# Kernel tuning notes

Measured on AMD Instinct MI355X. Metric: run time of the kernel, lower is better.

The kernel has to match this reference:

```python
import jax, jax.numpy as jnp
import numpy as np

B, S, D, H = 2, 2048, 1024, 16
DH = D // H

def setup_inputs() -> dict:
    key = jax.random.key(0)
    ks = jax.random.split(key, 9)
    s = 1.0 / np.sqrt(D)
    def lin(k):
        kw, kb = jax.random.split(k)
        W = jax.random.uniform(kw, (D, D), jnp.float32, -s, s)
        b = jax.random.uniform(kb, (D,), jnp.float32, -s, s)
        return W, b
    Wq, bq = lin(ks[0]); Wk, bk = lin(ks[1]); Wv, bv = lin(ks[2]); Wo, bo = lin(ks[3])
    x = jax.random.normal(ks[4], (B, S, D), jnp.float32)
    return {"x": x, "Wq": Wq, "bq": bq, "Wk": Wk, "bk": bk,
            "Wv": Wv, "bv": bv, "Wo": Wo, "bo": bo}

def _split_heads(t):
    # [B,S,D] -> [B,H,S,DH]
    return t.reshape(B, S, H, DH).transpose(0, 2, 1, 3)

def reference(x, Wq, bq, Wk, bk, Wv, bv, Wo, bo):
    # torch Linear: y = x @ W.T + b
    q = _split_heads(x @ Wq.T + bq)
    k = _split_heads(x @ Wk.T + bk)
    v = _split_heads(x @ Wv.T + bv)
    scores = jnp.einsum('bhqd,bhkd->bhqk', q, k) / jnp.sqrt(jnp.float32(DH))
    p = jax.nn.softmax(scores, axis=-1)  # dropout is identity in eval
    o = jnp.einsum('bhqk,bhkd->bhqd', p, v)
    o = o.transpose(0, 2, 1, 3).reshape(B, S, D)  # combine heads
    return o @ Wo.T + bo
```

## Files before the change

kernel.cpp:

```cpp
#include <hip/hip_runtime.h>


typedef __bf16 bf16;
typedef bf16 bf16x8 __attribute__((ext_vector_type(8)));
typedef bf16 bf16x4 __attribute__((ext_vector_type(4)));
typedef short s16x4 __attribute__((ext_vector_type(4)));
typedef float f32x4 __attribute__((ext_vector_type(4)));

#define MFMA32(a, b, c) __builtin_amdgcn_mfma_f32_16x16x32_bf16(a, b, c, 0, 0, 0)

#if __has_builtin(__builtin_amdgcn_mfma_f32_16x16x16bf16_1k)
#define HAVE_MFMA16 1
#define MFMA16(a, b, c) __builtin_amdgcn_mfma_f32_16x16x16bf16_1k(a, b, c, 0, 0, 0)
#else
#define HAVE_MFMA16 0
#endif

#define GLL(g, l) __builtin_amdgcn_global_load_lds(                              \
    (const __attribute__((address_space(1))) void*)(const void*)(g),             \
    (__attribute__((address_space(3))) void*)(void*)(l), 16, 0, 0)

union pk4 { bf16x4 h; s16x4 s; unsigned int d[2]; };

__global__ __launch_bounds__(256)
void cvt_bf16(const float* __restrict__ x,  const float* __restrict__ Wq,
              const float* __restrict__ Wk, const float* __restrict__ Wv,
              const float* __restrict__ Wo,
              bf16* __restrict__ xb, bf16* __restrict__ wqb, bf16* __restrict__ wkb,
              bf16* __restrict__ wvb, bf16* __restrict__ wob)
{
    const int idx = blockIdx.x * 256 + threadIdx.x;
    const float* src; bf16* dst; int off;
    if (idx < 1048576) { src = x; dst = xb; off = idx; }
    else {
        const int r = idx - 1048576;
        const int seg = r >> 18;
        off = r & 262143;
        src = (seg == 0) ? Wq : (seg == 1) ? Wk : (seg == 2) ? Wv : Wo;
        dst = (seg == 0) ? wqb : (seg == 1) ? wkb : (seg == 2) ? wvb : wob;
    }
    const float4 v = ((const float4*)src)[off];
    bf16x4 o = {(bf16)v.x, (bf16)v.y, (bf16)v.z, (bf16)v.w};
    *(bf16x4*)(dst + (size_t)off * 4) = o;
}

__global__ __launch_bounds__(256, 3)
void qkv_gemm(const bf16* __restrict__ xb,
              const bf16* __restrict__ wqb, const float* __restrict__ bq,
              const bf16* __restrict__ wkb, const float* __restrict__ bk,
              const bf16* __restrict__ wvb, const float* __restrict__ bv,
              bf16* __restrict__ q_ws, bf16* __restrict__ k_ws, bf16* __restrict__ v_ws)
{
    const int z = blockIdx.z;
    const bf16*  W    = (z == 0) ? wqb : (z == 1) ? wkb : wvb;
    const float* bias = (z == 0) ? bq  : (z == 1) ? bk  : bv;

    __shared__ bf16 As[128][64];
    __shared__ bf16 Bs[128][64];
    __shared__ char ebuf[17408];
    bf16 (*Et)[68]  = (bf16(*)[68])ebuf;
    bf16 (*Vt)[132] = (bf16(*)[132])ebuf;

    const int m0 = blockIdx.x * 128;
    const int n0 = blockIdx.y * 128;
    const int t    = threadIdx.x;
    const int wave = t >> 6;
    const int lane = t & 63;
    const int lr   = lane & 15;
    const int quad = lane >> 4;
    const int wm = (wave & 1) * 64;
    const int wn = (wave >> 1) * 64;

    const int srow8 = lane >> 3;
    const int pcol  = (lane & 7) * 8;
    const int gcol  = ((lane & 7) ^ (lane >> 3)) * 8;
    const bf16* gaU[4]; const bf16* gbU[4]; bf16* laU[4]; bf16* lbU[4];
    #pragma unroll
    for (int u = 0; u < 4; u++) {
        const int row = wave * 32 + u * 8 + srow8;
        gaU[u] = xb + (size_t)(m0 + row) * 1024 + gcol;
        gbU[u] = W  + (size_t)(n0 + row) * 1024 + gcol;
        laU[u] = &As[row][pcol];
        lbU[u] = &Bs[row][pcol];
    }
    const int swA = (lr & 7) * 8;

    f32x4 acc[4][4] = {};

    for (int k0 = 0; k0 < 1024; k0 += 64) {
        #pragma unroll
        for (int u = 0; u < 4; u++) {
            GLL(gaU[u] + k0, laU[u]);
            GLL(gbU[u] + k0, lbU[u]);
        }
        __syncthreads();

        bf16x8 af[4][2], bfr[4][2];
        #pragma unroll
        for (int i = 0; i < 4; i++)
            #pragma unroll
            for (int kc = 0; kc < 2; kc++)
                af[i][kc] = *(const bf16x8*)&As[wm + i*16 + lr][(kc*32 + quad*8) ^ swA];
        #pragma unroll
        for (int j = 0; j < 4; j++)
            #pragma unroll
            for (int kc = 0; kc < 2; kc++)
                bfr[j][kc] = *(const bf16x8*)&Bs[wn + j*16 + lr][(kc*32 + quad*8) ^ swA];
        #pragma unroll
        for (int kc = 0; kc < 2; kc++)
            #pragma unroll
            for (int i = 0; i < 4; i++)
                #pragma unroll
                for (int j = 0; j < 4; j++)
                    acc[i][j] = MFMA32(af[i][kc], bfr[j][kc], acc[i][j]);
        __syncthreads();
    }

    const int bi = m0 >> 11, si0 = m0 & 2047;
    if (z < 2) {
        bf16* hw = (z == 0) ? q_ws : k_ws;
        const float sc = (z == 0) ? 0.125f : 1.0f;
        #pragma unroll
        for (int ph = 0; ph < 2; ph++) {
            if ((wave >> 1) == ph) {
                #pragma unroll
                for (int j = 0; j < 4; j++) {
                    const float bb = bias[n0 + ph * 64 + j * 16 + lr];
                    #pragma unroll
                    for (int i = 0; i < 4; i++)
                        #pragma unroll
                        for (int r = 0; r < 4; r++)
                            Et[wm + i*16 + quad*4 + r][j*16 + lr] =
                                (bf16)((acc[i][j][r] + bb) * sc);
                }
            }
            __syncthreads();
            const int hh = (n0 >> 6) + ph;
            bf16* dst = hw + (((size_t)bi * 16 + hh) * 2048 + si0) * 64;
            const int row = t >> 1, cc = (t & 1) * 32;
            #pragma unroll
            for (int e = 0; e < 4; e++)
                *(bf16x8*)(dst + (size_t)row * 64 + cc + e * 8) =
                    *(const bf16x8*)&Et[row][cc + e * 8];
            __syncthreads();
        }
    } else {
        #pragma unroll
        for (int ph = 0; ph < 2; ph++) {
            if ((wave >> 1) == ph) {
                #pragma unroll
                for (int j = 0; j < 4; j++) {
                    const float bb = bias[n0 + ph * 64 + j * 16 + lr];
                    #pragma unroll
                    for (int i = 0; i < 4; i++)
                        #pragma unroll
                        for (int r = 0; r < 4; r++)
                            Vt[j * 16 + lr][wm + i * 16 + quad * 4 + r] =
                                (bf16)(acc[i][j][r] + bb);
                }
            }
            __syncthreads();
            const int c  = t >> 2;
            const int sc_ = (t & 3) * 32;
            const int col = n0 + ph * 64 + c;
            const int h = col >> 6, dh = col & 63;
            bf16* dst = v_ws + (((size_t)bi * 16 + h) * 64 + dh) * 2048 + si0 + sc_;
            #pragma unroll
            for (int e = 0; e < 4; e++)
                *(bf16x8*)(dst + e * 8) = *(const bf16x8*)&Vt[c][sc_ + e * 8];
            __syncthreads();
        }
    }
}

__global__ __launch_bounds__(512, 4)
void attn(const bf16* __restrict__ q_ws, const bf16* __restrict__ k_ws,
          const bf16* __restrict__ v_ws, bf16* __restrict__ o_ws)
{
    const int bh = blockIdx.x;
    const int qt = blockIdx.y;
    const int b_ = bh >> 4, h = bh & 15;

    const bf16* qbase = q_ws + (size_t)bh * 2048 * 64;
    const bf16* kbase = k_ws + (size_t)bh * 2048 * 64;
    const bf16* vbase = v_ws + (size_t)bh * 64 * 2048;

    __shared__ bf16 Ks[128][72];
    __shared__ bf16 Vs[64][140];

    const int t    = threadIdx.x;
    const int wave = t >> 6;
    const int lane = t & 63;
    const int lr   = lane & 15;
    const int quad = lane >> 4;

    bf16x8 aq[2];
    #pragma unroll
    for (int kc = 0; kc < 2; kc++)
        aq[kc] = *(const bf16x8*)(qbase +
            (size_t)(qt*128 + wave*16 + lr) * 64 + kc*32 + quad*8);

    float m_i = -1e30f, l_i = 0.f;
    f32x4 o_accT[4] = {};
    const float C = 1.44269504f;

    bf16x8 kreg[2], vreg[2];
    #pragma unroll
    for (int u = 0; u < 2; u++) {
        const int c = t + u * 512;
        kreg[u] = *(const bf16x8*)(kbase + (size_t)c * 8);
        vreg[u] = *(const bf16x8*)(vbase + (size_t)(c >> 4) * 2048 + (c & 15) * 8);
    }

    for (int kt = 0; kt < 16; kt++) {
        __syncthreads();
        #pragma unroll
        for (int u = 0; u < 2; u++) {
            const int c = t + u * 512;
            *(bf16x8*)&Ks[c >> 3][(c & 7) * 8]  = kreg[u];
            *(bf16x8*)&Vs[c >> 4][(c & 15) * 8] = vreg[u];
        }
        __syncthreads();
        if (kt < 15) {
            #pragma unroll
            for (int u = 0; u < 2; u++) {
                const int c = t + u * 512;
                kreg[u] = *(const bf16x8*)(kbase + (size_t)(kt+1) * 8192 + c * 8);
                vreg[u] = *(const bf16x8*)(vbase + (size_t)(c >> 4) * 2048
                                           + (kt+1) * 128 + (c & 15) * 8);
            }
        }

        f32x4 sacc[8];
        #pragma unroll
        for (int j = 0; j < 8; j++) {
            bf16x8 kf0 = *(const bf16x8*)&Ks[j*16 + lr][quad*8];
            bf16x8 kf1 = *(const bf16x8*)&Ks[j*16 + lr][32 + quad*8];
            f32x4 a = {0.f, 0.f, 0.f, 0.f};
            a = MFMA32(kf0, aq[0], a);
            a = MFMA32(kf1, aq[1], a);
            sacc[j] = a;
        }

        float m = -1e30f;
        #pragma unroll
        for (int j = 0; j < 8; j++)
            #pragma unroll
            for (int r = 0; r < 4; r++) m = fmaxf(m, sacc[j][r]);
        m = fmaxf(m, __shfl_xor(m, 16));
        m = fmaxf(m, __shfl_xor(m, 32));
        const float nm = fmaxf(m_i, m);
        const float al = exp2f((m_i - nm) * C);
        m_i = nm;
        const float nmc = nm * C;
        float rs = 0.f;
        #pragma unroll
        for (int j = 0; j < 8; j++)
            #pragma unroll
            for (int r = 0; r < 4; r++) {
                const float p = exp2f(fmaf(sacc[j][r], C, -nmc));
                sacc[j][r] = p;
                rs += p;
            }
        #pragma unroll
        for (int n = 0; n < 4; n++)
            #pragma unroll
            for (int r = 0; r < 4; r++) o_accT[n][r] *= al;
        rs += __shfl_xor(rs, 16);
        rs += __shfl_xor(rs, 32);
        l_i = l_i * al + rs;

#if HAVE_MFMA16
        #pragma unroll
        for (int j = 0; j < 8; j++) {
            pk4 pf;
            pf.h = bf16x4{(bf16)sacc[j][0], (bf16)sacc[j][1],
                          (bf16)sacc[j][2], (bf16)sacc[j][3]};
            #pragma unroll
            for (int fb = 0; fb < 4; fb++) {
                pk4 vf;
                *(unsigned long long*)vf.d =
                    *(const unsigned long long*)&Vs[fb*16 + lr][j*16 + quad*4];
                o_accT[fb] = MFMA16(vf.s, pf.s, o_accT[fb]);
            }
        }
#else
        unsigned int p0[8], p1[8];
        #pragma unroll
        for (int j = 0; j < 8; j++) {
            pk4 pf;
            pf.h = bf16x4{(bf16)sacc[j][0], (bf16)sacc[j][1],
                          (bf16)sacc[j][2], (bf16)sacc[j][3]};
            p0[j] = pf.d[0]; p1[j] = pf.d[1];
        }
        const int srcA = lr + 32 * (quad & 1);
        const int srcB = srcA + 16;
        const bool hi = (quad >> 1) != 0;
        #pragma unroll
        for (int c = 0; c < 4; c++) {
            unsigned int a0 = __shfl(p0[2*c], srcA), a1 = __shfl(p0[2*c+1], srcA);
            unsigned int b0 = __shfl(p1[2*c], srcA), b1 = __shfl(p1[2*c+1], srcA);
            unsigned int c0 = __shfl(p0[2*c], srcB), c1 = __shfl(p0[2*c+1], srcB);
            unsigned int d0 = __shfl(p1[2*c], srcB), d1 = __shfl(p1[2*c+1], srcB);
            unsigned int fr[4];
            fr[0] = hi ? a1 : a0;
            fr[1] = hi ? b1 : b0;
            fr[2] = hi ? c1 : c0;
            fr[3] = hi ? d1 : d0;
            bf16x8 pf8 = *(bf16x8*)fr;
            #pragma unroll
            for (int fb = 0; fb < 4; fb++) {
                bf16x8 vf8 = *(const bf16x8*)&Vs[fb*16 + lr][c*32 + quad*8];
                o_accT[fb] = MFMA32(vf8, pf8, o_accT[fb]);
            }
        }
#endif
    }

    __syncthreads();
    bf16 (*OsE)[68] = (bf16(*)[68])&Ks[0][0];
    const float inv = 1.0f / l_i;
    const int sil = wave * 16 + lr;
    #pragma unroll
    for (int fb = 0; fb < 4; fb++)
        #pragma unroll
        for (int r = 0; r < 4; r++)
            OsE[sil][fb*16 + quad*4 + r] = (bf16)(o_accT[fb][r] * inv);
    __syncthreads();
    const int row = t >> 2, seg = (t & 3) * 16;
    bf16* dst = o_ws + ((size_t)b_ * 2048 + qt*128 + row) * 1024 + h*64 + seg;
    *(bf16x8*)(dst)     = *(const bf16x8*)&OsE[row][seg];
    *(bf16x8*)(dst + 8) = *(const bf16x8*)&OsE[row][seg + 8];
}

__global__ __launch_bounds__(256, 3)
void out_gemm(const bf16* __restrict__ o_ws,
              const bf16* __restrict__ wob, const float* __restrict__ bo,
              float* __restrict__ out)
{
    __shared__ bf16 As[64][64];
    __shared__ bf16 Bs[128][64];
    __shared__ float Ot[64][68];

    const int m0 = blockIdx.x * 64;
    const int n0 = blockIdx.y * 128;
    const int t    = threadIdx.x;
    const int wave = t >> 6;
    const int lane = t & 63;
    const int lr   = lane & 15;
    const int quad = lane >> 4;
    const int wm = (wave & 1) * 32;
    const int wn = (wave >> 1) * 64;

    const int srow8 = lane >> 3;
    const int pcol  = (lane & 7) * 8;
    const int gcol  = ((lane & 7) ^ (lane >> 3)) * 8;
    const bf16* gaU[2]; bf16* laU[2];
    #pragma unroll
    for (int u = 0; u < 2; u++) {
        const int row = wave * 16 + u * 8 + srow8;
        gaU[u] = o_ws + (size_t)(m0 + row) * 1024 + gcol;
        laU[u] = &As[row][pcol];
    }
    const bf16* gbU[4]; bf16* lbU[4];
    #pragma unroll
    for (int u = 0; u < 4; u++) {
        const int row = wave * 32 + u * 8 + srow8;
        gbU[u] = wob + (size_t)(n0 + row) * 1024 + gcol;
        lbU[u] = &Bs[row][pcol];
    }
    const int swA = (lr & 7) * 8;

    f32x4 acc[2][4] = {};

    for (int k0 = 0; k0 < 1024; k0 += 64) {
        #pragma unroll
        for (int u = 0; u < 2; u++) GLL(gaU[u] + k0, laU[u]);
        #pragma unroll
        for (int u = 0; u < 4; u++) GLL(gbU[u] + k0, lbU[u]);
        __syncthreads();

        bf16x8 af[2][2], bfr[4][2];
        #pragma unroll
        for (int i = 0; i < 2; i++)
            #pragma unroll
            for (int kc = 0; kc < 2; kc++)
                af[i][kc] = *(const bf16x8*)&As[wm + i*16 + lr][(kc*32 + quad*8) ^ swA];
        #pragma unroll
        for (int j = 0; j < 4; j++)
            #pragma unroll
            for (int kc = 0; kc < 2; kc++)
                bfr[j][kc] = *(const bf16x8*)&Bs[wn + j*16 + lr][(kc*32 + quad*8) ^ swA];
        #pragma unroll
        for (int kc = 0; kc < 2; kc++)
            #pragma unroll
            for (int i = 0; i < 2; i++)
                #pragma unroll
                for (int j = 0; j < 4; j++)
                    acc[i][j] = MFMA32(af[i][kc], bfr[j][kc], acc[i][j]);
        __syncthreads();
    }

    #pragma unroll
    for (int ph = 0; ph < 2; ph++) {
        if ((wave >> 1) == ph) {
            #pragma unroll
            for (int j = 0; j < 4; j++) {
                const float bb = bo[n0 + ph * 64 + j * 16 + lr];
                #pragma unroll
                for (int i = 0; i < 2; i++)
                    #pragma unroll
                    for (int r = 0; r < 4; r++)
                        Ot[wm + i*16 + quad*4 + r][j*16 + lr] = acc[i][j][r] + bb;
            }
        }
        __syncthreads();
        const int row = t >> 2, seg = (t & 3) * 16;
        float* dst = out + (size_t)(m0 + row) * 1024 + n0 + ph * 64 + seg;
        #pragma unroll
        for (int e = 0; e < 4; e++)
            *(float4*)(dst + e * 4) = *(const float4*)&Ot[row][seg + e * 4];
        __syncthreads();
    }
}

extern "C" void kernel_launch(void* const* d_in, const int* in_sizes, int n_in,
                              void* d_out, int out_size, void* d_ws, size_t ws_size,
                              hipStream_t stream) {
    (void)in_sizes; (void)n_in; (void)out_size; (void)ws_size;
    const float* x  = (const float*)d_in[0];
    const float* Wq = (const float*)d_in[1];
    const float* bq = (const float*)d_in[2];
    const float* Wk = (const float*)d_in[3];
    const float* bk = (const float*)d_in[4];
    const float* Wv = (const float*)d_in[5];
    const float* bv = (const float*)d_in[6];
    const float* Wo = (const float*)d_in[7];
    const float* bo = (const float*)d_in[8];
    float* out = (float*)d_out;

    char* ws = (char*)d_ws;
    const size_t MB = 1024 * 1024;
    bf16* xb   = (bf16*)(ws);
    bf16* wqb  = (bf16*)(ws + 8 * MB);
    bf16* wkb  = (bf16*)(ws + 10 * MB);
    bf16* wvb  = (bf16*)(ws + 12 * MB);
    bf16* wob  = (bf16*)(ws + 14 * MB);
    bf16* q_ws = (bf16*)(ws + 16 * MB);
    bf16* k_ws = (bf16*)(ws + 24 * MB);
    bf16* v_ws = (bf16*)(ws + 32 * MB);
    bf16* o_ws = (bf16*)(ws + 40 * MB);

    hipLaunchKernelGGL(cvt_bf16, dim3(8192), dim3(256), 0, stream,
                       x, Wq, Wk, Wv, Wo, xb, wqb, wkb, wvb, wob);
    hipLaunchKernelGGL(qkv_gemm, dim3(32, 8, 3), dim3(256), 0, stream,
                       xb, wqb, bq, wkb, bk, wvb, bv, q_ws, k_ws, v_ws);
    hipLaunchKernelGGL(attn, dim3(32, 16), dim3(512), 0, stream,
                       q_ws, k_ws, v_ws, o_ws);
    hipLaunchKernelGGL(out_gemm, dim3(64, 8), dim3(256), 0, stream,
                       o_ws, wob, bo, out);
}
```

Measured before the change: 212.7 us.

## Double query rows per wave and double-buffer K/V tiles in attention

Each wave now handles two 16-row query subtiles, so every K/V fragment read from LDS feeds twice as many MFMAs. The attention grid shrinks to 8 query tiles of 256 rows. K/V LDS staging is double-buffered with register prefetch two tiles ahead, which drops one barrier per iteration. In exchange it doubles accumulator registers and LDS use, lowers launch-bounds occupancy to 2, and halves the number of blocks (256), which may underfill the GPU.

```diff
diff --git a/kernel.cpp b/kernel.cpp
--- a/kernel.cpp
+++ b/kernel.cpp
@@ -173,7 +173,7 @@
     }
 }
 
-__global__ __launch_bounds__(512, 4)
+__global__ __launch_bounds__(512, 2)
 void attn(const bf16* __restrict__ q_ws, const bf16* __restrict__ k_ws,
           const bf16* __restrict__ v_ws, bf16* __restrict__ o_ws)
 {
@@ -185,8 +185,8 @@
     const bf16* kbase = k_ws + (size_t)bh * 2048 * 64;
     const bf16* vbase = v_ws + (size_t)bh * 64 * 2048;
 
-    __shared__ bf16 Ks[128][72];
-    __shared__ bf16 Vs[64][140];
+    __shared__ bf16 KsB[2 * 128 * 72];
+    __shared__ bf16 VsB[2 * 64 * 140];
 
     const int t    = threadIdx.x;
     const int wave = t >> 6;
@@ -194,143 +194,171 @@
     const int lr   = lane & 15;
     const int quad = lane >> 4;
 
-    bf16x8 aq[2];
-    #pragma unroll
-    for (int kc = 0; kc < 2; kc++)
-        aq[kc] = *(const bf16x8*)(qbase +
-            (size_t)(qt*128 + wave*16 + lr) * 64 + kc*32 + quad*8);
-
-    float m_i = -1e30f, l_i = 0.f;
-    f32x4 o_accT[4] = {};
+    bf16x8 aq[2][2];
+    #pragma unroll
+    for (int s = 0; s < 2; s++)
+        #pragma unroll
+        for (int kc = 0; kc < 2; kc++)
+            aq[s][kc] = *(const bf16x8*)(qbase +
+                (size_t)(qt*256 + wave*32 + s*16 + lr) * 64 + kc*32 + quad*8);
+
+    float m_i[2] = {-1e30f, -1e30f}, l_i[2] = {0.f, 0.f};
+    f32x4 o_accT[2][4] = {};
     const float C = 1.44269504f;
 
+    const int c0 = t, c1 = t + 512;
     bf16x8 kreg[2], vreg[2];
-    #pragma unroll
-    for (int u = 0; u < 2; u++) {
-        const int c = t + u * 512;
-        kreg[u] = *(const bf16x8*)(kbase + (size_t)c * 8);
-        vreg[u] = *(const bf16x8*)(vbase + (size_t)(c >> 4) * 2048 + (c & 15) * 8);
-    }
+
+    #define LOADREGS(kt_)                                                         \
+        kreg[0] = *(const bf16x8*)(kbase + (size_t)(kt_) * 8192 + c0 * 8);        \
+        kreg[1] = *(const bf16x8*)(kbase + (size_t)(kt_) * 8192 + c1 * 8);        \
+        vreg[0] = *(const bf16x8*)(vbase + (size_t)(c0 >> 4) * 2048 + (kt_) * 128 \
+                                   + (c0 & 15) * 8);                              \
+        vreg[1] = *(const bf16x8*)(vbase + (size_t)(c1 >> 4) * 2048 + (kt_) * 128 \
+                                   + (c1 & 15) * 8);
+
+    #define STAGE(p_)                                                             \
+        *(bf16x8*)&KsB[(p_) * 9216 + (c0 >> 3) * 72 + (c0 & 7) * 8]  = kreg[0];   \
+        *(bf16x8*)&KsB[(p_) * 9216 + (c1 >> 3) * 72 + (c1 & 7) * 8]  = kreg[1];   \
+        *(bf16x8*)&VsB[(p_) * 8960 + (c0 >> 4) * 140 + (c0 & 15) * 8] = vreg[0];  \
+        *(bf16x8*)&VsB[(p_) * 8960 + (c1 >> 4) * 140 + (c1 & 15) * 8] = vreg[1];
+
+    LOADREGS(0);
+    STAGE(0);
+    LOADREGS(1);
+    __syncthreads();
 
     for (int kt = 0; kt < 16; kt++) {
-        __syncthreads();
-        #pragma unroll
-        for (int u = 0; u < 2; u++) {
-            const int c = t + u * 512;
-            *(bf16x8*)&Ks[c >> 3][(c & 7) * 8]  = kreg[u];
-            *(bf16x8*)&Vs[c >> 4][(c & 15) * 8] = vreg[u];
-        }
-        __syncthreads();
-        if (kt < 15) {
-            #pragma unroll
-            for (int u = 0; u < 2; u++) {
-                const int c = t + u * 512;
-                kreg[u] = *(const bf16x8*)(kbase + (size_t)(kt+1) * 8192 + c * 8);
-                vreg[u] = *(const bf16x8*)(vbase + (size_t)(c >> 4) * 2048
-                                           + (kt+1) * 128 + (c & 15) * 8);
-            }
-        }
-
-        f32x4 sacc[8];
+        const int p = kt & 1;
+        if (kt < 15) { STAGE(p ^ 1); }
+        if (kt < 14) { LOADREGS(kt + 2); }
+        const bf16* Ksp = &KsB[p * 9216];
+        const bf16* Vsp = &VsB[p * 8960];
+
+        f32x4 sacc[2][8];
         #pragma unroll
         for (int j = 0; j < 8; j++) {
-            bf16x8 kf0 = *(const bf16x8*)&Ks[j*16 + lr][quad*8];
-            bf16x8 kf1 = *(const bf16x8*)&Ks[j*16 + lr][32 + quad*8];
-            f32x4 a = {0.f, 0.f, 0.f, 0.f};
-            a = MFMA32(kf0, aq[0], a);
-            a = MFMA32(kf1, aq[1], a);
-            sacc[j] = a;
-        }
-
-        float m = -1e30f;
-        #pragma unroll
-        for (int j = 0; j < 8; j++)
-            #pragma unroll
-            for (int r = 0; r < 4; r++) m = fmaxf(m, sacc[j][r]);
-        m = fmaxf(m, __shfl_xor(m, 16));
-        m = fmaxf(m, __shfl_xor(m, 32));
-        const float nm = fmaxf(m_i, m);
-        const float al = exp2f((m_i - nm) * C);
-        m_i = nm;
-        const float nmc = nm * C;
-        float rs = 0.f;
-        #pragma unroll
-        for (int j = 0; j < 8; j++)
-            #pragma unroll
-            for (int r = 0; r < 4; r++) {
-                const float p = exp2f(fmaf(sacc[j][r], C, -nmc));
-                sacc[j][r] = p;
-                rs += p;
-            }
-        #pragma unroll
-        for (int n = 0; n < 4; n++)
-            #pragma unroll
-            for (int r = 0; r < 4; r++) o_accT[n][r] *= al;
-        rs += __shfl_xor(rs, 16);
-        rs += __shfl_xor(rs, 32);
-        l_i = l_i * al + rs;
+            bf16x8 kf0 = *(const bf16x8*)&Ksp[(j*16 + lr) * 72 + quad*8];
+            bf16x8 kf1 = *(const bf16x8*)&Ksp[(j*16 + lr) * 72 + 32 + quad*8];
+            #pragma unroll
+            for (int s = 0; s < 2; s++) {
+                f32x4 a = {0.f, 0.f, 0.f, 0.f};
+                a = MFMA32(kf0, aq[s][0], a);
+                a = MFMA32(kf1, aq[s][1], a);
+                sacc[s][j] = a;
+            }
+        }
+
+        #pragma unroll
+        for (int s = 0; s < 2; s++) {
+            float m = -1e30f;
+            #pragma unroll
+            for (int j = 0; j < 8; j++)
+                #pragma unroll
+                for (int r = 0; r < 4; r++) m = fmaxf(m, sacc[s][j][r]);
+            m = fmaxf(m, __shfl_xor(m, 16));
+            m = fmaxf(m, __shfl_xor(m, 32));
+            const float nm = fmaxf(m_i[s], m);
+            const float al = exp2f((m_i[s] - nm) * C);
+            m_i[s] = nm;
+            const float nmc = nm * C;
+            float rs = 0.f;
+            #pragma unroll
+            for (int j = 0; j < 8; j++)
+                #pragma unroll
+                for (int r = 0; r < 4; r++) {
+                    const float pv = exp2f(fmaf(sacc[s][j][r], C, -nmc));
+                    sacc[s][j][r] = pv;
+                    rs += pv;
+                }
+            #pragma unroll
+            for (int n = 0; n < 4; n++)
+                #pragma unroll
+                for (int r = 0; r < 4; r++) o_accT[s][n][r] *= al;
+            rs += __shfl_xor(rs, 16);
+            rs += __shfl_xor(rs, 32);
+            l_i[s] = l_i[s] * al + rs;
+        }
 
 #if HAVE_MFMA16
         #pragma unroll
         for (int j = 0; j < 8; j++) {
-            pk4 pf;
-            pf.h = bf16x4{(bf16)sacc[j][0], (bf16)sacc[j][1],
-                          (bf16)sacc[j][2], (bf16)sacc[j][3]};
+            pk4 pf0, pf1;
+            pf0.h = bf16x4{(bf16)sacc[0][j][0], (bf16)sacc[0][j][1],
+                           (bf16)sacc[0][j][2], (bf16)sacc[0][j][3]};
+            pf1.h = bf16x4{(bf16)sacc[1][j][0], (bf16)sacc[1][j][1],
+                           (bf16)sacc[1][j][2], (bf16)sacc[1][j][3]};
             #pragma unroll
             for (int fb = 0; fb < 4; fb++) {
                 pk4 vf;
-                *(unsigned long long*)vf.d =
-                    *(const unsigned long long*)&Vs[fb*16 + lr][j*16 + quad*4];
-                o_accT[fb] = MFMA16(vf.s, pf.s, o_accT[fb]);
+                *(unsigned long long*)vf.d = *(const unsigned long long*)
+                    &Vsp[(fb*16 + lr) * 140 + j*16 + quad*4];
+                o_accT[0][fb] = MFMA16(vf.s, pf0.s, o_accT[0][fb]);
+                o_accT[1][fb] = MFMA16(vf.s, pf1.s, o_accT[1][fb]);
             }
         }
 #else
-        unsigned int p0[8], p1[8];
-        #pragma unroll
-        for (int j = 0; j < 8; j++) {
-            pk4 pf;
-            pf.h = bf16x4{(bf16)sacc[j][0], (bf16)sacc[j][1],
-                          (bf16)sacc[j][2], (bf16)sacc[j][3]};
-            p0[j] = pf.d[0]; p1[j] = pf.d[1];
-        }
-        const int srcA = lr + 32 * (quad & 1);
-        const int srcB = srcA + 16;
-        const bool hi = (quad >> 1) != 0;
-        #pragma unroll
-        for (int c = 0; c < 4; c++) {
-            unsigned int a0 = __shfl(p0[2*c], srcA), a1 = __shfl(p0[2*c+1], srcA);
-            unsigned int b0 = __shfl(p1[2*c], srcA), b1 = __shfl(p1[2*c+1], srcA);
-            unsigned int c0 = __shfl(p0[2*c], srcB), c1 = __shfl(p0[2*c+1], srcB);
-            unsigned int d0 = __shfl(p1[2*c], srcB), d1 = __shfl(p1[2*c+1], srcB);
-            unsigned int fr[4];
-            fr[0] = hi ? a1 : a0;
-            fr[1] = hi ? b1 : b0;
-            fr[2] = hi ? c1 : c0;
-            fr[3] = hi ? d1 : d0;
-            bf16x8 pf8 = *(bf16x8*)fr;
-            #pragma unroll
-            for (int fb = 0; fb < 4; fb++) {
-                bf16x8 vf8 = *(const bf16x8*)&Vs[fb*16 + lr][c*32 + quad*8];
-                o_accT[fb] = MFMA32(vf8, pf8, o_accT[fb]);
+        #pragma unroll
+        for (int s = 0; s < 2; s++) {
+            unsigned int p0[8], p1[8];
+            #pragma unroll
+            for (int j = 0; j < 8; j++) {
+                pk4 pf;
+                pf.h = bf16x4{(bf16)sacc[s][j][0], (bf16)sacc[s][j][1],
+                              (bf16)sacc[s][j][2], (bf16)sacc[s][j][3]};
+                p0[j] = pf.d[0]; p1[j] = pf.d[1];
+            }
+            const int srcA = lr + 32 * (quad & 1);
+            const int srcB = srcA + 16;
+            const bool hi = (quad >> 1) != 0;
+            #pragma unroll
+            for (int c = 0; c < 4; c++) {
+                unsigned int a0 = __shfl(p0[2*c], srcA), a1 = __shfl(p0[2*c+1], srcA);
+                unsigned int b0 = __shfl(p1[2*c], srcA), b1 = __shfl(p1[2*c+1], srcA);
+                unsigned int c0_ = __shfl(p0[2*c], srcB), c1_ = __shfl(p0[2*c+1], srcB);
+                unsigned int d0 = __shfl(p1[2*c], srcB), d1 = __shfl(p1[2*c+1], srcB);
+                unsigned int fr[4];
+                fr[0] = hi ? a1 : a0;
+                fr[1] = hi ? b1 : b0;
+                fr[2] = hi ? c1_ : c0_;
+                fr[3] = hi ? d1 : d0;
+                bf16x8 pf8 = *(bf16x8*)fr;
+                #pragma unroll
+                for (int fb = 0; fb < 4; fb++) {
+                    unsigned long long w0 = *(const unsigned long long*)
+                        &Vsp[(fb*16 + lr) * 140 + c*32 + quad*8];
+                    unsigned long long w1 = *(const unsigned long long*)
+                        &Vsp[(fb*16 + lr) * 140 + c*32 + quad*8 + 4];
+                    unsigned long long vv[2] = {w0, w1};
+                    bf16x8 vf8 = *(bf16x8*)vv;
+                    o_accT[s][fb] = MFMA32(vf8, pf8, o_accT[s][fb]);
+                }
             }
         }
 #endif
-    }
-
-    __syncthreads();
-    bf16 (*OsE)[68] = (bf16(*)[68])&Ks[0][0];
-    const float inv = 1.0f / l_i;
-    const int sil = wave * 16 + lr;
-    #pragma unroll
-    for (int fb = 0; fb < 4; fb++)
-        #pragma unroll
-        for (int r = 0; r < 4; r++)
-            OsE[sil][fb*16 + quad*4 + r] = (bf16)(o_accT[fb][r] * inv);
-    __syncthreads();
-    const int row = t >> 2, seg = (t & 3) * 16;
-    bf16* dst = o_ws + ((size_t)b_ * 2048 + qt*128 + row) * 1024 + h*64 + seg;
-    *(bf16x8*)(dst)     = *(const bf16x8*)&OsE[row][seg];
-    *(bf16x8*)(dst + 8) = *(const bf16x8*)&OsE[row][seg + 8];
+        __syncthreads();
+    }
+
+    bf16 (*OsE)[68] = (bf16(*)[68])&KsB[0];
+    #pragma unroll
+    for (int s = 0; s < 2; s++) {
+        const float inv = 1.0f / l_i[s];
+        const int sil = wave * 16 + lr;
+        #pragma unroll
+        for (int fb = 0; fb < 4; fb++)
+            #pragma unroll
+            for (int r = 0; r < 4; r++)
+                OsE[sil][fb*16 + quad*4 + r] = (bf16)(o_accT[s][fb][r] * inv);
+        __syncthreads();
+        const int row = t >> 2, seg = (t & 3) * 16;
+        const int grow = qt*256 + (row >> 4)*32 + s*16 + (row & 15);
+        bf16* dst = o_ws + ((size_t)b_ * 2048 + grow) * 1024 + h*64 + seg;
+        *(bf16x8*)(dst)     = *(const bf16x8*)&OsE[row][seg];
+        *(bf16x8*)(dst + 8) = *(const bf16x8*)&OsE[row][seg + 8];
+        if (s == 0) __syncthreads();
+    }
+    #undef LOADREGS
+    #undef STAGE
 }
 
 __global__ __launch_bounds__(256, 3)
@@ -455,7 +483,7 @@
                        x, Wq, Wk, Wv, Wo, xb, wqb, wkb, wvb, wob);
     hipLaunchKernelGGL(qkv_gemm, dim3(32, 8, 3), dim3(256), 0, stream,
                        xb, wqb, bq, wkb, bk, wvb, bv, q_ws, k_ws, v_ws);
-    hipLaunchKernelGGL(attn, dim3(32, 16), dim3(512), 0, stream,
+    hipLaunchKernelGGL(attn, dim3(32, 8), dim3(512), 0, stream,
                        q_ws, k_ws, v_ws, o_ws);
     hipLaunchKernelGGL(out_gemm, dim3(64, 8), dim3(256), 0, stream,
                        o_ws, wob, bo, out);
```

Result: faster. 204.4 us (-3.9%).
